# Performance work log

Hardware: AMD Instinct MI355X
Metric: run time of the kernel (lower is better)

Reference implementation:

```python
import jax, jax.numpy as jnp
import numpy as np

S, B, D, E = 257, 64, 768, 8
H = 4 * D  # expert hidden dim

def quick_gelu(x):
    return x * jax.nn.sigmoid(1.702 * x)

def setup_inputs() -> dict:
    key = jax.random.key(0)
    ks = jax.random.split(key, 7)
    scale = 1.0 / np.sqrt(D)
    return {
        "x": jax.random.normal(ks[0], (S, B, D), dtype=jnp.float32),
        "W1": jax.random.normal(ks[1], (E, H, D), dtype=jnp.float32) * scale,   # fc1 weight per expert (out,in)
        "b1": jax.random.normal(ks[2], (E, H), dtype=jnp.float32) * 0.01,
        "W2": jax.random.normal(ks[3], (E, D, H), dtype=jnp.float32) * (1.0 / np.sqrt(H)),
        "b2": jax.random.normal(ks[4], (E, D), dtype=jnp.float32) * 0.01,
        "Wr": jax.random.normal(ks[5], (E, D), dtype=jnp.float32) * scale,       # router weight (E, d)
        "br": jnp.zeros((E,), dtype=jnp.float32),
    }

def reference(x, W1, b1, W2, b2, Wr, br):
    s, b, d = x.shape
    xf = x.reshape(s * b, d)                                  # [T, d]
    logits = xf @ Wr.T + br                                   # [T, E]
    probs = jax.nn.softmax(logits, axis=-1)                   # [T, E]
    # all-experts MLP, batched over the expert axis
    h = jnp.einsum('td,ehd->teh', xf, W1) + b1                # [T, E, 4d]
    h = quick_gelu(h)
    outs = jnp.einsum('teh,edh->ted', h, W2) + b2             # [T, E, d]
    y = jnp.einsum('ted,te->td', outs, probs)                 # router-weighted combine
    return y.reshape(s, b, d)
```

## Files before the change

kernel.cpp:

```cpp
#include <hip/hip_runtime.h>

typedef unsigned short u16;
typedef float f32x4 __attribute__((ext_vector_type(4)));
typedef short s16x8 __attribute__((ext_vector_type(8)));

#define T_TOK   16448L
#define D_DIM   768L
#define H_DIM   3072L
#define E_NUM   8L
#define M_PAD   16640L

__device__ __forceinline__ u16 f2bf(float f){
  unsigned u = __float_as_uint(f);
  u = u + 0x7FFFu + ((u >> 16) & 1u);
  return (u16)(u >> 16);
}
__device__ __forceinline__ unsigned f2bf2(float a, float b){
  return (unsigned)f2bf(a) | ((unsigned)f2bf(b) << 16);
}

__device__ __forceinline__ void gload_lds16(const u16* g, u16* s){
  __builtin_amdgcn_global_load_lds((const __attribute__((address_space(1))) void*)g,
                                   (__attribute__((address_space(3))) void*)s,
                                   16, 0, 0);
}

__device__ __forceinline__ int xcd_chunk(int idx, int n){
  const int q = n >> 3, r = n & 7, x = idx & 7;
  return (x < r ? x*(q+1) : r*(q+1) + (x-r)*q) + (idx >> 3);
}

__global__ __launch_bounds__(256) void k_pro(const float* __restrict__ x,
                                             const float* __restrict__ W1,
                                             const float* __restrict__ W2,
                                             const float* __restrict__ Wr,
                                             const float* __restrict__ br,
                                             u16* __restrict__ xb,
                                             u16* __restrict__ w1b,
                                             u16* __restrict__ w2b,
                                             float* __restrict__ probs){
  const int bx = (int)blockIdx.x, tid = threadIdx.x;
  if (bx < 6240){
    const long base = ((long)bx*256 + tid) << 3;
    uint4 o;
    if (base < T_TOK*D_DIM){
      const float4 f0 = *(const float4*)(x + base);
      const float4 f1 = *(const float4*)(x + base + 4);
      o.x = f2bf2(f0.x, f0.y); o.y = f2bf2(f0.z, f0.w);
      o.z = f2bf2(f1.x, f1.y); o.w = f2bf2(f1.z, f1.w);
    } else { o.x = o.y = o.z = o.w = 0u; }
    *(uint4*)(xb + base) = o;
  } else if (bx < 24672){
    const int  wsel = (bx < 15456) ? 0 : 1;
    const long base = ((long)(bx - (wsel ? 15456 : 6240))*256 + tid) << 3;
    const float* src = wsel ? W2 : W1;
    u16* dst = wsel ? w2b : w1b;
    const float4 f0 = *(const float4*)(src + base);
    const float4 f1 = *(const float4*)(src + base + 4);
    uint4 o;
    o.x = f2bf2(f0.x, f0.y); o.y = f2bf2(f0.z, f0.w);
    o.z = f2bf2(f1.x, f1.y); o.w = f2bf2(f1.z, f1.w);
    *(uint4*)(dst + base) = o;
  } else {
    const int w = (int)(((long)(bx - 24672)*256 + tid) >> 6);
    const int lane = tid & 63;
    if (w >= (int)T_TOK) return;
    const float* xr = x + (long)w * D_DIM;
    float l[8];
#pragma unroll
    for (int e = 0; e < 8; ++e) l[e] = 0.f;
#pragma unroll
    for (int c = 0; c < 3; ++c){
      const float4 xv = *(const float4*)(xr + c*256 + lane*4);
#pragma unroll
      for (int e = 0; e < 8; ++e){
        const float4 wv = *(const float4*)(Wr + (long)e*D_DIM + c*256 + lane*4);
        l[e] += xv.x*wv.x + xv.y*wv.y + xv.z*wv.z + xv.w*wv.w;
      }
    }
#pragma unroll
    for (int e = 0; e < 8; ++e){
#pragma unroll
      for (int off = 32; off > 0; off >>= 1) l[e] += __shfl_xor(l[e], off);
      l[e] += br[e];
    }
    float m = l[0];
#pragma unroll
    for (int e = 1; e < 8; ++e) m = fmaxf(m, l[e]);
    float s = 0.f;
#pragma unroll
    for (int e = 0; e < 8; ++e){ l[e] = __expf(l[e] - m); s += l[e]; }
    const float inv = 1.f / s;
    if (lane == 0){
      float4 p0 = { l[0]*inv, l[1]*inv, l[2]*inv, l[3]*inv };
      float4 p1 = { l[4]*inv, l[5]*inv, l[6]*inv, l[7]*inv };
      *(float4*)(probs + (long)w*8)     = p0;
      *(float4*)(probs + (long)w*8 + 4) = p1;
    }
  }
}

#define FENCE()  __builtin_amdgcn_sched_barrier(0)
#define BAR()    do{ FENCE(); __builtin_amdgcn_s_barrier(); FENCE(); }while(0)
#define LGK0()   do{ asm volatile("s_waitcnt lgkmcnt(0)" ::: "memory"); FENCE(); }while(0)

__device__ __forceinline__ s16x8 ld_frag(const u16* S, int rbase, int c, int ln){
  const int r = rbase + ln;
  return *(const s16x8*)(S + (r << 6) + ((c ^ (r & 7)) << 3));
}

__device__ __forceinline__ void gemm256(const u16* __restrict__ Ag, long lda,
                                        const u16* __restrict__ Bg, long ldb,
                                        int NT, u16* lds, int tid,
                                        f32x4 (&acc)[8][4]){
  const int l  = tid & 63, w = tid >> 6;
  const int wr = w >> 2,  wc = w & 3;
  const int g4 = l >> 4,  ln = l & 15;

  const int rw = l >> 3;
  const int c8 = (l & 7) ^ rw;
  const u16* gA = Ag + (long)(w*8 + rw) * lda + c8*8;
  const u16* gB = Bg + (long)(w*8 + rw) * ldb + c8*8;
  u16* s0 = lds + w*512;
#define SA(par,T,rnd) gload_lds16(gA + (long)(T)*64 + (long)(rnd)*64*lda, s0 + (par)*32768 + (rnd)*4096)
#define SB(par,T,rnd) gload_lds16(gB + (long)(T)*64 + (long)(rnd)*64*ldb, s0 + (par)*32768 + 16384 + (rnd)*4096)

#pragma unroll
  for (int i = 0; i < 4; ++i) SA(0,0,i);
#pragma unroll
  for (int i = 0; i < 4; ++i) SB(0,0,i);
  SA(1,1,0); SB(1,1,0); SA(1,1,2); SB(1,1,1);
  FENCE();
  asm volatile("s_waitcnt vmcnt(4)" ::: "memory");
  BAR();

  for (int kt = 0; kt < NT; ++kt){
    const int par = kt & 1, oth = par ^ 1;
    const u16* As = lds + par * 32768;
    const u16* Bs = As + 16384;
    const bool st1 = (kt + 1 < NT), st2 = (kt + 2 < NT);
    s16x8 aL[4], aH[4], b0[4], b1[4];

#pragma unroll
    for (int ni = 0; ni < 4; ++ni) b0[ni] = ld_frag(Bs, wc*64 + ni*16, g4, ln);
#pragma unroll
    for (int mi = 0; mi < 4; ++mi) aL[mi] = ld_frag(As, wr*128 + mi*16, g4, ln);
    if (st1){ SA(oth, kt+1, 1); SB(oth, kt+1, 2); }
    BAR(); LGK0();
    __builtin_amdgcn_s_setprio(1);
#pragma unroll
    for (int mi = 0; mi < 4; ++mi)
#pragma unroll
      for (int ni = 0; ni < 4; ++ni)
        acc[mi][ni] = __builtin_amdgcn_mfma_f32_16x16x32_bf16(aL[mi], b0[ni], acc[mi][ni], 0, 0, 0);
    __builtin_amdgcn_s_setprio(0);
    BAR();

#pragma unroll
    for (int ni = 0; ni < 4; ++ni) b1[ni] = ld_frag(Bs, wc*64 + ni*16, 4 + g4, ln);
#pragma unroll
    for (int mi = 0; mi < 4; ++mi) aL[mi] = ld_frag(As, wr*128 + mi*16, 4 + g4, ln);
    if (st1){ SA(oth, kt+1, 3); SB(oth, kt+1, 3); }
    BAR(); LGK0();
    __builtin_amdgcn_s_setprio(1);
#pragma unroll
    for (int mi = 0; mi < 4; ++mi)
#pragma unroll
      for (int ni = 0; ni < 4; ++ni)
        acc[mi][ni] = __builtin_amdgcn_mfma_f32_16x16x32_bf16(aL[mi], b1[ni], acc[mi][ni], 0, 0, 0);
    __builtin_amdgcn_s_setprio(0);
    BAR();

#pragma unroll
    for (int mi = 0; mi < 4; ++mi) aH[mi] = ld_frag(As, wr*128 + 64 + mi*16, g4, ln);
    if (st2){ SA(par, kt+2, 0); SB(par, kt+2, 0); }
    BAR(); LGK0();
    __builtin_amdgcn_s_setprio(1);
#pragma unroll
    for (int mi = 0; mi < 4; ++mi)
#pragma unroll
      for (int ni = 0; ni < 4; ++ni)
        acc[mi+4][ni] = __builtin_amdgcn_mfma_f32_16x16x32_bf16(aH[mi], b0[ni], acc[mi+4][ni], 0, 0, 0);
    __builtin_amdgcn_s_setprio(0);
    BAR();

#pragma unroll
    for (int mi = 0; mi < 4; ++mi) aH[mi] = ld_frag(As, wr*128 + 64 + mi*16, 4 + g4, ln);
    if (st2){ SA(par, kt+2, 2); SB(par, kt+2, 1); }
    BAR(); LGK0();
    __builtin_amdgcn_s_setprio(1);
#pragma unroll
    for (int mi = 0; mi < 4; ++mi)
#pragma unroll
      for (int ni = 0; ni < 4; ++ni)
        acc[mi+4][ni] = __builtin_amdgcn_mfma_f32_16x16x32_bf16(aH[mi], b1[ni], acc[mi+4][ni], 0, 0, 0);
    __builtin_amdgcn_s_setprio(0);

    if (st1){
      FENCE();
      if (st2) asm volatile("s_waitcnt vmcnt(4)" ::: "memory");
      else     asm volatile("s_waitcnt vmcnt(0)" ::: "memory");
      BAR();
    }
  }
#undef SA
#undef SB
}

__global__ __launch_bounds__(512, 2) void k_pair(const u16* __restrict__ xb,
                                                 const u16* __restrict__ w1b,
                                                 const float* __restrict__ b1,
                                                 const u16* __restrict__ w2b,
                                                 const float* __restrict__ b2,
                                                 const float* __restrict__ probs,
                                                 float* __restrict__ out,
                                                 const u16* __restrict__ hbR,
                                                 u16* __restrict__ hbW,
                                                 int e2, int t02,
                                                 int e1, int t01, int mt1, int n2){
  __shared__ alignas(16) u16 lds[65536];
  const int tid = threadIdx.x;
  const int l  = tid & 63, w = tid >> 6;
  const int wr = w >> 2,  wc = w & 3;
  const int g4 = l >> 4,  ln = l & 15;
  const int bx = (int)blockIdx.x;
  f32x4 acc[8][4] = {};

  if (bx < n2){
    const int wg = xcd_chunk(bx, n2);
    const int tx = wg / 3, ty = wg % 3;
    const int m0 = tx << 8, n0 = ty << 8;
    gemm256(hbR + (long)m0 * H_DIM, H_DIM,
            w2b + ((long)e2 * D_DIM + n0) * H_DIM, H_DIM,
            48, lds, tid, acc);
    float bias[4];
#pragma unroll
    for (int ni = 0; ni < 4; ++ni) bias[ni] = b2[(long)e2*D_DIM + n0 + wc*64 + ni*16 + ln];
#pragma unroll
    for (int mi = 0; mi < 8; ++mi){
#pragma unroll
      for (int j = 0; j < 4; ++j){
        const int gt = t02 + m0 + wr*128 + mi*16 + g4*4 + j;
        if (gt < (int)T_TOK){
          const float p = probs[(long)gt*8 + e2];
          float* dst = out + (long)gt * D_DIM + n0 + wc*64;
#pragma unroll
          for (int ni = 0; ni < 4; ++ni){
            const float v = p * (acc[mi][ni][j] + bias[ni]);
            if (e2 == 0) dst[ni*16 + ln] = v;
            else         dst[ni*16 + ln] += v;
          }
        }
      }
    }
  } else {
    const int n1 = (int)gridDim.x - n2;
    const int wg = xcd_chunk(bx - n2, n1);
    const int tx = wg % mt1, ty = wg / mt1;
    const int m0 = tx << 8, n0 = ty << 8;
    gemm256(xb + (long)(t01 + m0) * D_DIM, D_DIM,
            w1b + ((long)e1 * H_DIM + n0) * D_DIM, D_DIM,
            12, lds, tid, acc);
    float bias[4];
#pragma unroll
    for (int ni = 0; ni < 4; ++ni) bias[ni] = b1[(long)e1*H_DIM + n0 + wc*64 + ni*16 + ln];
#pragma unroll
    for (int mi = 0; mi < 8; ++mi){
#pragma unroll
      for (int j = 0; j < 4; ++j){
        const int r = m0 + wr*128 + mi*16 + g4*4 + j;
        u16* dst = hbW + (long)r * H_DIM + n0 + wc*64;
#pragma unroll
        for (int ni = 0; ni < 4; ++ni){
          const float v  = acc[mi][ni][j] + bias[ni];
          const float gl = v / (1.0f + __expf(-1.702f * v));
          dst[ni*16 + ln] = f2bf(gl);
        }
      }
    }
  }
}

__global__ __launch_bounds__(512, 2) void k_g2split(const u16* __restrict__ w2b,
                                                    const float* __restrict__ b2,
                                                    const float* __restrict__ probs,
                                                    float* __restrict__ out,
                                                    const u16* __restrict__ hbR,
                                                    int e2, int t02, int n2){
  __shared__ alignas(16) u16 lds[65536];
  const int tid = threadIdx.x;
  const int l  = tid & 63, w = tid >> 6;
  const int wr = w >> 2,  wc = w & 3;
  const int g4 = l >> 4,  ln = l & 15;
  f32x4 acc[8][4] = {};

  const int wg = xcd_chunk((int)blockIdx.x, n2);
  const int ty = wg % 3;
  const int sp = (wg / 3) & 1;
  const int tx = wg / 6;
  const int m0 = tx << 8, n0 = ty << 8;
  gemm256(hbR + (long)m0 * H_DIM + sp*1536, H_DIM,
          w2b + ((long)e2 * D_DIM + n0) * H_DIM + sp*1536, H_DIM,
          24, lds, tid, acc);
  float bias[4];
#pragma unroll
  for (int ni = 0; ni < 4; ++ni)
    bias[ni] = (sp == 0) ? b2[(long)e2*D_DIM + n0 + wc*64 + ni*16 + ln] : 0.f;
#pragma unroll
  for (int mi = 0; mi < 8; ++mi){
#pragma unroll
    for (int j = 0; j < 4; ++j){
      const int gt = t02 + m0 + wr*128 + mi*16 + g4*4 + j;
      if (gt < (int)T_TOK){
        const float p = probs[(long)gt*8 + e2];
        float* dst = out + (long)gt * D_DIM + n0 + wc*64;
#pragma unroll
        for (int ni = 0; ni < 4; ++ni)
          atomicAdd(&dst[ni*16 + ln], p * (acc[mi][ni][j] + bias[ni]));
      }
    }
  }
}

extern "C" void kernel_launch(void* const* d_in, const int* in_sizes, int n_in,
                              void* d_out, int out_size, void* d_ws, size_t ws_size,
                              hipStream_t stream){
  const float* x  = (const float*)d_in[0];
  const float* W1 = (const float*)d_in[1];
  const float* b1 = (const float*)d_in[2];
  const float* W2 = (const float*)d_in[3];
  const float* b2 = (const float*)d_in[4];
  const float* Wr = (const float*)d_in[5];
  const float* br = (const float*)d_in[6];
  float* out = (float*)d_out;

  char* ws = (char*)d_ws;
  size_t off = 0;
  auto carve = [&](size_t bytes)->void*{
    void* p = ws + off; off += (bytes + 255) & ~(size_t)255; return p;
  };
  u16*   xb    = (u16*)  carve((size_t)M_PAD * D_DIM * 2);
  u16*   w1b   = (u16*)  carve((size_t)E_NUM * H_DIM * D_DIM * 2);
  u16*   w2b   = (u16*)  carve((size_t)E_NUM * D_DIM * H_DIM * 2);
  float* probs = (float*)carve((size_t)T_TOK * E_NUM * 4);
  u16*   hbA   = (u16*)  carve((size_t)8192 * H_DIM * 2);
  u16*   hbB   = (u16*)  carve((size_t)8448 * H_DIM * 2);

  k_pro<<<dim3(28784), dim3(256), 0, stream>>>(x, W1, W2, Wr, br, xb, w1b, w2b, probs);

  const int MTA = 32, MTB = 33;
  const int T0A = 0,  T0B = 8192;

  auto pair = [&](int e2, const u16* hbR, int t02, int mt2,
                  int e1, u16* hbW, int t01, int mt1){
    const int n2 = mt2 * 3;
    const int n1 = mt1 * 12;
    k_pair<<<dim3((unsigned)(n2 + n1)), dim3(512), 0, stream>>>(
        xb, w1b, b1, w2b, b2, probs, out, hbR, hbW,
        e2, t02, e1, t01, mt1, n2);
  };

  pair(0, nullptr, 0, 0, 0, hbA, T0A, MTA);
  for (int e = 0; e < 8; ++e){
    pair(e, hbA, T0A, MTA, e, hbB, T0B, MTB);
    if (e < 7) pair(e, hbB, T0B, MTB, e + 1, hbA, T0A, MTA);
  }
  k_g2split<<<dim3((unsigned)(MTB * 6)), dim3(512), 0, stream>>>(
      w2b, b2, probs, out, hbB, 7, T0B, MTB * 6);
}
```

Baseline: 1.964 ms.

## Replace double-buffered interleaved GEMM pipeline with simple single-buffer load-sync-compute loop

The hand-scheduled double-buffered main loop, which issued global-to-LDS prefetches two k-tiles ahead and interleaved them with four MFMA phases under explicit barriers, wait counts and priority hints, is replaced. The new loop loads one k-tile into a single LDS buffer, synchronises, runs all MFMAs, then synchronises again. LDS use per block halves, which may allow more co-resident blocks, but global loads no longer overlap with compute. Both the pair kernel and the split-K kernel now use the smaller shared buffer.

New measurement: 2.522 ms. 28.4% more time.

```diff
diff --git a/kernel.cpp b/kernel.cpp
--- a/kernel.cpp
+++ b/kernel.cpp
@@ -100,10 +100,6 @@
   }
 }
 
-#define FENCE()  __builtin_amdgcn_sched_barrier(0)
-#define BAR()    do{ FENCE(); __builtin_amdgcn_s_barrier(); FENCE(); }while(0)
-#define LGK0()   do{ asm volatile("s_waitcnt lgkmcnt(0)" ::: "memory"); FENCE(); }while(0)
-
 __device__ __forceinline__ s16x8 ld_frag(const u16* S, int rbase, int c, int ln){
   const int r = rbase + ln;
   return *(const s16x8*)(S + (r << 6) + ((c ^ (r & 7)) << 3));
@@ -119,92 +115,47 @@
 
   const int rw = l >> 3;
   const int c8 = (l & 7) ^ rw;
-  const u16* gA = Ag + (long)(w*8 + rw) * lda + c8*8;
-  const u16* gB = Bg + (long)(w*8 + rw) * ldb + c8*8;
-  u16* s0 = lds + w*512;
-#define SA(par,T,rnd) gload_lds16(gA + (long)(T)*64 + (long)(rnd)*64*lda, s0 + (par)*32768 + (rnd)*4096)
-#define SB(par,T,rnd) gload_lds16(gB + (long)(T)*64 + (long)(rnd)*64*ldb, s0 + (par)*32768 + 16384 + (rnd)*4096)
-
-#pragma unroll
-  for (int i = 0; i < 4; ++i) SA(0,0,i);
-#pragma unroll
-  for (int i = 0; i < 4; ++i) SB(0,0,i);
-  SA(1,1,0); SB(1,1,0); SA(1,1,2); SB(1,1,1);
-  FENCE();
-  asm volatile("s_waitcnt vmcnt(4)" ::: "memory");
-  BAR();
+  const u16* pA = Ag + (long)(w*8 + rw) * lda + c8*8;
+  const u16* pB = Bg + (long)(w*8 + rw) * ldb + c8*8;
+  const long sA = 64 * lda, sB = 64 * ldb;
+  u16* dA = lds + w*512;
+  u16* dB = lds + 16384 + w*512;
 
   for (int kt = 0; kt < NT; ++kt){
-    const int par = kt & 1, oth = par ^ 1;
-    const u16* As = lds + par * 32768;
-    const u16* Bs = As + 16384;
-    const bool st1 = (kt + 1 < NT), st2 = (kt + 2 < NT);
-    s16x8 aL[4], aH[4], b0[4], b1[4];
-
+    gload_lds16(pA,        dA);
+    gload_lds16(pA +   sA, dA + 4096);
+    gload_lds16(pA + 2*sA, dA + 8192);
+    gload_lds16(pA + 3*sA, dA + 12288);
+    gload_lds16(pB,        dB);
+    gload_lds16(pB +   sB, dB + 4096);
+    gload_lds16(pB + 2*sB, dB + 8192);
+    gload_lds16(pB + 3*sB, dB + 12288);
+    pA += 64; pB += 64;
+    __syncthreads();
+
+    const u16* As = lds;
+    const u16* Bs = lds + 16384;
+    s16x8 a0[8], b0[4], a1[8], b1[4];
 #pragma unroll
     for (int ni = 0; ni < 4; ++ni) b0[ni] = ld_frag(Bs, wc*64 + ni*16, g4, ln);
 #pragma unroll
-    for (int mi = 0; mi < 4; ++mi) aL[mi] = ld_frag(As, wr*128 + mi*16, g4, ln);
-    if (st1){ SA(oth, kt+1, 1); SB(oth, kt+1, 2); }
-    BAR(); LGK0();
-    __builtin_amdgcn_s_setprio(1);
-#pragma unroll
-    for (int mi = 0; mi < 4; ++mi)
+    for (int mi = 0; mi < 8; ++mi) a0[mi] = ld_frag(As, wr*128 + mi*16, g4, ln);
+#pragma unroll
+    for (int mi = 0; mi < 8; ++mi)
 #pragma unroll
       for (int ni = 0; ni < 4; ++ni)
-        acc[mi][ni] = __builtin_amdgcn_mfma_f32_16x16x32_bf16(aL[mi], b0[ni], acc[mi][ni], 0, 0, 0);
-    __builtin_amdgcn_s_setprio(0);
-    BAR();
-
+        acc[mi][ni] = __builtin_amdgcn_mfma_f32_16x16x32_bf16(a0[mi], b0[ni], acc[mi][ni], 0, 0, 0);
 #pragma unroll
     for (int ni = 0; ni < 4; ++ni) b1[ni] = ld_frag(Bs, wc*64 + ni*16, 4 + g4, ln);
 #pragma unroll
-    for (int mi = 0; mi < 4; ++mi) aL[mi] = ld_frag(As, wr*128 + mi*16, 4 + g4, ln);
-    if (st1){ SA(oth, kt+1, 3); SB(oth, kt+1, 3); }
-    BAR(); LGK0();
-    __builtin_amdgcn_s_setprio(1);
-#pragma unroll
-    for (int mi = 0; mi < 4; ++mi)
+    for (int mi = 0; mi < 8; ++mi) a1[mi] = ld_frag(As, wr*128 + mi*16, 4 + g4, ln);
+#pragma unroll
+    for (int mi = 0; mi < 8; ++mi)
 #pragma unroll
       for (int ni = 0; ni < 4; ++ni)
-        acc[mi][ni] = __builtin_amdgcn_mfma_f32_16x16x32_bf16(aL[mi], b1[ni], acc[mi][ni], 0, 0, 0);
-    __builtin_amdgcn_s_setprio(0);
-    BAR();
-
-#pragma unroll
-    for (int mi = 0; mi < 4; ++mi) aH[mi] = ld_frag(As, wr*128 + 64 + mi*16, g4, ln);
-    if (st2){ SA(par, kt+2, 0); SB(par, kt+2, 0); }
-    BAR(); LGK0();
-    __builtin_amdgcn_s_setprio(1);
-#pragma unroll
-    for (int mi = 0; mi < 4; ++mi)
-#pragma unroll
-      for (int ni = 0; ni < 4; ++ni)
-        acc[mi+4][ni] = __builtin_amdgcn_mfma_f32_16x16x32_bf16(aH[mi], b0[ni], acc[mi+4][ni], 0, 0, 0);
-    __builtin_amdgcn_s_setprio(0);
-    BAR();
-
-#pragma unroll
-    for (int mi = 0; mi < 4; ++mi) aH[mi] = ld_frag(As, wr*128 + 64 + mi*16, 4 + g4, ln);
-    if (st2){ SA(par, kt+2, 2); SB(par, kt+2, 1); }
-    BAR(); LGK0();
-    __builtin_amdgcn_s_setprio(1);
-#pragma unroll
-    for (int mi = 0; mi < 4; ++mi)
-#pragma unroll
-      for (int ni = 0; ni < 4; ++ni)
-        acc[mi+4][ni] = __builtin_amdgcn_mfma_f32_16x16x32_bf16(aH[mi], b1[ni], acc[mi+4][ni], 0, 0, 0);
-    __builtin_amdgcn_s_setprio(0);
-
-    if (st1){
-      FENCE();
-      if (st2) asm volatile("s_waitcnt vmcnt(4)" ::: "memory");
-      else     asm volatile("s_waitcnt vmcnt(0)" ::: "memory");
-      BAR();
-    }
-  }
-#undef SA
-#undef SB
+        acc[mi][ni] = __builtin_amdgcn_mfma_f32_16x16x32_bf16(a1[mi], b1[ni], acc[mi][ni], 0, 0, 0);
+    __syncthreads();
+  }
 }
 
 __global__ __launch_bounds__(512, 2) void k_pair(const u16* __restrict__ xb,
@@ -218,7 +169,7 @@
                                                  u16* __restrict__ hbW,
                                                  int e2, int t02,
                                                  int e1, int t01, int mt1, int n2){
-  __shared__ alignas(16) u16 lds[65536];
+  __shared__ alignas(16) u16 lds[32768];
   const int tid = threadIdx.x;
   const int l  = tid & 63, w = tid >> 6;
   const int wr = w >> 2,  wc = w & 3;
@@ -287,7 +238,7 @@
                                                     float* __restrict__ out,
                                                     const u16* __restrict__ hbR,
                                                     int e2, int t02, int n2){
-  __shared__ alignas(16) u16 lds[65536];
+  __shared__ alignas(16) u16 lds[32768];
   const int tid = threadIdx.x;
   const int l  = tid & 63, w = tid >> 6;
   const int wr = w >> 2,  wc = w & 3;
```
